# Kernel optimization log

Measured on AMD Instinct MI355X. Metric: run time of the kernel, lower is better.

Reference implementation:

```python
import jax, jax.numpy as jnp
import numpy as np

C, N, B = 16, 65536, 4096  # cases, points per case, batch of case IDs


def _w(key, fan_in, fan_out):
    return jax.random.normal(key, (fan_in, fan_out), dtype=jnp.float32) / np.sqrt(fan_in).astype(np.float32)


def setup_inputs() -> dict:
    key = jax.random.key(0)
    ks = jax.random.split(key, 8)
    pts = jax.random.normal(ks[0], (C, N, 3), dtype=jnp.float32)
    inp = {
        "pts": pts,
        "W1_0": _w(ks[1], 3, 64), "b1_0": jnp.zeros((64,), jnp.float32),
        "W1_1": _w(ks[2], 64, 128), "b1_1": jnp.zeros((128,), jnp.float32),
        "W1_2": _w(ks[3], 128, 512), "b1_2": jnp.zeros((512,), jnp.float32),
        "W2_0": _w(ks[4], 512, 256), "b2_0": jnp.zeros((256,), jnp.float32),
        "W2_1": _w(ks[5], 256, 512), "b2_1": jnp.zeros((512,), jnp.float32),
        "x": jax.random.randint(ks[6], (B,), 0, C, dtype=jnp.int64),
    }
    return inp


def reference(pts, W1_0, b1_0, W1_1, b1_1, W1_2, b1_2, W2_0, b2_0, W2_1, b2_1, x):
    def mlp1(h):  # shared per-point MLP, SiLU after every layer
        h = jax.nn.silu(h @ W1_0 + b1_0)
        h = jax.nn.silu(h @ W1_1 + b1_1)
        h = jax.nn.silu(h @ W1_2 + b1_2)
        return h

    feats = mlp1(pts)                       # [C, N, F1]
    idx = jnp.argmax(feats, axis=1)         # [C, F1] critical-point indices per feature
    # gather critical points (detached in the torch original)
    fixed = jax.lax.stop_gradient(pts[jnp.arange(pts.shape[0])[:, None], idx])  # [C, F1, 3]

    feats2 = mlp1(fixed)                    # [C, F1, F1]
    latent0 = jnp.max(feats2, axis=1)       # [C, F1]

    h = jax.nn.silu(latent0 @ W2_0 + b2_0)  # [C, 256]
    latent = h @ W2_1 + b2_1                # [C, total_modes*ge_features]

    caseID_unit = jax.nn.one_hot(x, latent.shape[0], dtype=latent.dtype)  # [B, C]
    return caseID_unit @ latent             # [B, 512]
```

## Files before the change

### kernel.cpp

```cpp
#include <hip/hip_runtime.h>
#include <math.h>

#define NCASES   16
#define NPTS_BIG 65536
#define F1       512
#define OUT_B    4096

typedef __attribute__((ext_vector_type(8))) short  short8;
typedef __attribute__((ext_vector_type(4))) float  floatx4;

__device__ __forceinline__ float silu_f(float x) {
    return x * __builtin_amdgcn_rcpf(1.0f + __expf(-x));
}

__device__ __forceinline__ unsigned short f2bf(float x) {
    unsigned u = __float_as_uint(x);
    u += 0x7FFFu + ((u >> 16) & 1u);
    return (unsigned short)(u >> 16);
}

__device__ __forceinline__ unsigned enc_f(float x) {
    unsigned u = __float_as_uint(x);
    return (u & 0x80000000u) ? ~u : (u | 0x80000000u);
}
__device__ __forceinline__ float dec_f(unsigned e) {
    unsigned u = (e & 0x80000000u) ? (e ^ 0x80000000u) : ~e;
    return __uint_as_float(u);
}

__global__ void k_init_u64(unsigned long long* a, int n) {
    int i = blockIdx.x * blockDim.x + threadIdx.x;
    if (i < n) a[i] = 0ull;
}

__global__ void k_prep(const float* __restrict__ W11, const float* __restrict__ W12,
                       unsigned short* __restrict__ BbWs, unsigned short* __restrict__ BcWs)
{
    int i = blockIdx.x * 256 + threadIdx.x;
    if (i < 65536) {
        int j = i & 7, l = (i >> 3) & 63, t = i >> 9;
        int KT = t & 3, NT = (t >> 2) & 3, w = t >> 4;
        int k = KT * 32 + (l >> 4) * 8 + j;
        int f = w * 64 + NT * 16 + (l & 15);
        BcWs[i] = f2bf(W12[(size_t)k * 512 + f]);
    }
    if (i < 8192) {
        int j = i & 7, l = (i >> 3) & 63, t = i >> 9;
        int KT = t & 1, w = t >> 1;
        int k = KT * 32 + (l >> 4) * 8 + j;
        int f = w * 16 + (l & 15);
        BbWs[i] = f2bf(W11[(size_t)k * 128 + f]);
    }
}

__global__ __launch_bounds__(512, 2)
void k_mlp1_argmax(const float* __restrict__ pts, int nPts, int chunksPerBlock,
                   const float* __restrict__ W10, const float* __restrict__ b10,
                   const float* __restrict__ b11, const float* __restrict__ b12,
                   const unsigned short* __restrict__ BbWs,
                   const unsigned short* __restrict__ BcWs,
                   unsigned long long* __restrict__ argOut)
{
    const int c   = blockIdx.y;
    const int tid = threadIdx.x;
    const int w   = tid >> 6;
    const int l   = tid & 63;
    const int lm  = l & 15;
    const int q   = l >> 4;

    __shared__ float s_w10[3][64];
    __shared__ float s_b10v[64];
    __shared__ __align__(16) unsigned short s_h0[64][72];
    __shared__ __align__(16) unsigned short s_h1[64][136];

    if (tid < 192) ((float*)s_w10)[tid] = W10[tid];
    if (tid < 64)  s_b10v[tid] = b10[tid];

    short8 Bc[16];
    #pragma unroll
    for (int t = 0; t < 16; ++t)
        Bc[t] = *(const short8*)(BcWs + (size_t)((w * 16 + t) * 64 + l) * 8);
    short8 Bb[2];
    #pragma unroll
    for (int t = 0; t < 2; ++t)
        Bb[t] = *(const short8*)(BbWs + (size_t)((w * 2 + t) * 64 + l) * 8);

    const float bias11 = b11[w * 16 + lm];
    float bias12[4];
    #pragma unroll
    for (int NT = 0; NT < 4; ++NT) bias12[NT] = b12[w * 64 + NT * 16 + lm];

    float    bestv[4];
    unsigned besti[4];
    #pragma unroll
    for (int NT = 0; NT < 4; ++NT) { bestv[NT] = -INFINITY; besti[NT] = 0u; }

    const float* cpts = pts + (size_t)c * nPts * 3;

    for (int ch = 0; ch < chunksPerBlock; ++ch) {
        const int pbase = (blockIdx.x * chunksPerBlock + ch) * 64;
        __syncthreads();

        {
            const int p = tid >> 3, f0 = (tid & 7) * 8;
            const float x = cpts[(size_t)(pbase + p) * 3 + 0];
            const float y = cpts[(size_t)(pbase + p) * 3 + 1];
            const float z = cpts[(size_t)(pbase + p) * 3 + 2];
            short8 hv;
            #pragma unroll
            for (int jj = 0; jj < 8; ++jj) {
                const int f = f0 + jj;
                float v = x * s_w10[0][f] + y * s_w10[1][f] + z * s_w10[2][f] + s_b10v[f];
                hv[jj] = (short)f2bf(silu_f(v));
            }
            *(short8*)&s_h0[p][f0] = hv;
        }
        __syncthreads();

        #pragma unroll
        for (int MT = 0; MT < 4; ++MT) {
            short8 a0 = *(const short8*)&s_h0[MT * 16 + lm][q * 8];
            short8 a1 = *(const short8*)&s_h0[MT * 16 + lm][32 + q * 8];
            floatx4 acc = {0.f, 0.f, 0.f, 0.f};
            acc = __builtin_amdgcn_mfma_f32_16x16x32_bf16(a0, Bb[0], acc, 0, 0, 0);
            acc = __builtin_amdgcn_mfma_f32_16x16x32_bf16(a1, Bb[1], acc, 0, 0, 0);
            #pragma unroll
            for (int r = 0; r < 4; ++r)
                s_h1[MT * 16 + q * 4 + r][w * 16 + lm] = f2bf(silu_f(acc[r] + bias11));
        }
        __syncthreads();

        #pragma unroll
        for (int MT = 0; MT < 4; ++MT) {
            short8 a[4];
            #pragma unroll
            for (int KT = 0; KT < 4; ++KT)
                a[KT] = *(const short8*)&s_h1[MT * 16 + lm][KT * 32 + q * 8];
            #pragma unroll
            for (int NT = 0; NT < 4; ++NT) {
                floatx4 acc = {0.f, 0.f, 0.f, 0.f};
                #pragma unroll
                for (int KT = 0; KT < 4; ++KT)
                    acc = __builtin_amdgcn_mfma_f32_16x16x32_bf16(a[KT], Bc[NT * 4 + KT], acc, 0, 0, 0);
                #pragma unroll
                for (int r = 0; r < 4; ++r) {
                    float v = acc[r];
                    if (v > bestv[NT]) {
                        bestv[NT] = v;
                        besti[NT] = (unsigned)(pbase + MT * 16 + q * 4 + r);
                    }
                }
            }
        }
    }

    #pragma unroll
    for (int NT = 0; NT < 4; ++NT) {
        float v = bestv[NT]; unsigned i = besti[NT];
        #pragma unroll
        for (int m = 16; m <= 32; m <<= 1) {
            float    vo = __shfl_xor(v, m, 64);
            unsigned io = __shfl_xor(i, m, 64);
            if (vo > v || (vo == v && io < i)) { v = vo; i = io; }
        }
        if (q == 0) {
            v += bias12[NT];
            unsigned long long key = ((unsigned long long)enc_f(v) << 32)
                                   | (unsigned long long)(~i);
            atomicMax(&argOut[(size_t)c * 512 + w * 64 + NT * 16 + lm], key);
        }
    }
}

__global__ void k_gather(const float* __restrict__ pts,
                         const unsigned long long* __restrict__ argBuf,
                         float* __restrict__ fixedPts, int nPts)
{
    int id = blockIdx.x * blockDim.x + threadIdx.x;
    if (id >= NCASES * F1) return;
    int c = id >> 9;
    unsigned idx = ~(unsigned)(argBuf[id] & 0xFFFFFFFFull);
    const float* src = pts + ((size_t)c * nPts + idx) * 3;
    float* dst = fixedPts + (size_t)id * 3;
    dst[0] = src[0]; dst[1] = src[1]; dst[2] = src[2];
}

__global__ __launch_bounds__(256)
void k_head(const unsigned long long* __restrict__ argBuf2,
            const float* __restrict__ W20, const float* __restrict__ b20,
            const float* __restrict__ W21, const float* __restrict__ b21,
            float* __restrict__ latent)
{
    const int c = blockIdx.x, tid = threadIdx.x;
    __shared__ float l0[512];
    __shared__ float hh[256];
    l0[tid]       = silu_f(dec_f((unsigned)(argBuf2[(size_t)c * 512 + tid] >> 32)));
    l0[tid + 256] = silu_f(dec_f((unsigned)(argBuf2[(size_t)c * 512 + tid + 256] >> 32)));
    __syncthreads();
    float acc = b20[tid];
    for (int k = 0; k < 512; ++k) acc += l0[k] * W20[(size_t)k * 256 + tid];
    hh[tid] = silu_f(acc);
    __syncthreads();
    #pragma unroll
    for (int r = 0; r < 2; ++r) {
        int f = tid + r * 256;
        float a2 = b21[f];
        for (int k = 0; k < 256; ++k) a2 += hh[k] * W21[(size_t)k * 512 + f];
        latent[(size_t)c * 512 + f] = a2;
    }
}

__global__ void k_scatter(const int* __restrict__ x,
                          const float* __restrict__ latent,
                          float* __restrict__ out)
{
    const int b = blockIdx.x, t = threadIdx.x;
    int cid = x[b];
    const float4* src = (const float4*)(latent + (size_t)cid * 512);
    float4* dst = (float4*)(out + (size_t)b * 512);
    dst[t] = src[t];
}

extern "C" void kernel_launch(void* const* d_in, const int* in_sizes, int n_in,
                              void* d_out, int out_size, void* d_ws, size_t ws_size,
                              hipStream_t stream)
{
    const float* pts = (const float*)d_in[0];
    const float* W10 = (const float*)d_in[1];
    const float* b10 = (const float*)d_in[2];
    const float* W11 = (const float*)d_in[3];
    const float* b11 = (const float*)d_in[4];
    const float* W12 = (const float*)d_in[5];
    const float* b12 = (const float*)d_in[6];
    const float* W20 = (const float*)d_in[7];
    const float* b20 = (const float*)d_in[8];
    const float* W21 = (const float*)d_in[9];
    const float* b21 = (const float*)d_in[10];
    const int*   x   = (const int*)d_in[11];
    float* out = (float*)d_out;

    char* ws = (char*)d_ws;
    unsigned long long* argBuf  = (unsigned long long*)ws;
    unsigned long long* argBuf2 = (unsigned long long*)(ws + 65536);
    float* fixedPts             = (float*)(ws + 131072);
    float* latent               = (float*)(ws + 229376);
    unsigned short* BbWs        = (unsigned short*)(ws + 262144);
    unsigned short* BcWs        = (unsigned short*)(ws + 278528);

    k_init_u64<<<dim3(64), dim3(256), 0, stream>>>(argBuf, NCASES * F1 * 2);

    k_prep<<<dim3(256), dim3(256), 0, stream>>>(W11, W12, BbWs, BcWs);

    k_mlp1_argmax<<<dim3(128, NCASES), dim3(512), 0, stream>>>(
        pts, NPTS_BIG, 8, W10, b10, b11, b12, BbWs, BcWs, argBuf);

    k_gather<<<dim3(32), dim3(256), 0, stream>>>(pts, argBuf, fixedPts, NPTS_BIG);

    k_mlp1_argmax<<<dim3(8, NCASES), dim3(512), 0, stream>>>(
        fixedPts, F1, 1, W10, b10, b11, b12, BbWs, BcWs, argBuf2);

    k_head<<<dim3(NCASES), dim3(256), 0, stream>>>(argBuf2, W20, b20, W21, b21, latent);

    k_scatter<<<dim3(OUT_B), dim3(128), 0, stream>>>(x, latent, out);
}
```

Before: 285.1 us.

## Pack argmax index into mantissa bits, fuse gather and init, use SGPR layer-0 weights

The per-element compare-and-select argmax in the hot loop becomes a plain fmax chain. The low 7 mantissa bits of each accumulator are overwritten with an encoded chunk/row position, and the index is decoded after the loop. The separate gather and init kernels are removed: the second MLP pass reads critical points by index directly, and the argmax buffers are zeroed inside k_prep. Layer-0 weights are held per wave as scalar (uniform) values instead of in LDS, bf16 packing uses a perm instruction, bias11 is preloaded into the MFMA accumulator, and one barrier per chunk is dropped. Truncating 7 mantissa bits slightly coarsens value comparisons, which can change argmax selection between near-tied candidates.

```diff
diff --git a/kernel.cpp b/kernel.cpp
--- a/kernel.cpp
+++ b/kernel.cpp
@@ -13,10 +13,15 @@
     return x * __builtin_amdgcn_rcpf(1.0f + __expf(-x));
 }
 
+__device__ __forceinline__ unsigned f2bf_hi(float x) {
+    unsigned u = __float_as_uint(x);
+    return u + 0x7FFFu + ((u >> 16) & 1u);
+}
 __device__ __forceinline__ unsigned short f2bf(float x) {
-    unsigned u = __float_as_uint(x);
-    u += 0x7FFFu + ((u >> 16) & 1u);
-    return (unsigned short)(u >> 16);
+    return (unsigned short)(f2bf_hi(x) >> 16);
+}
+__device__ __forceinline__ unsigned pk2bf(float lo, float hi) {
+    return __builtin_amdgcn_perm(f2bf_hi(hi), f2bf_hi(lo), 0x07060302u);
 }
 
 __device__ __forceinline__ unsigned enc_f(float x) {
@@ -28,16 +33,17 @@
     return __uint_as_float(u);
 }
 
-__global__ void k_init_u64(unsigned long long* a, int n) {
-    int i = blockIdx.x * blockDim.x + threadIdx.x;
-    if (i < n) a[i] = 0ull;
+__device__ __forceinline__ float sgpr_f(float x) {
+    return __uint_as_float(__builtin_amdgcn_readfirstlane(__float_as_uint(x)));
 }
 
 __global__ void k_prep(const float* __restrict__ W11, const float* __restrict__ W12,
-                       unsigned short* __restrict__ BbWs, unsigned short* __restrict__ BcWs)
+                       unsigned short* __restrict__ BbWs, unsigned short* __restrict__ BcWs,
+                       unsigned long long* __restrict__ argBufs)
 {
     int i = blockIdx.x * 256 + threadIdx.x;
-    if (i < 65536) {
+    if (i < 16384) argBufs[i] = 0ull;
+    {
         int j = i & 7, l = (i >> 3) & 63, t = i >> 9;
         int KT = t & 3, NT = (t >> 2) & 3, w = t >> 4;
         int k = KT * 32 + (l >> 4) * 8 + j;
@@ -55,6 +61,7 @@
 
 __global__ __launch_bounds__(512, 2)
 void k_mlp1_argmax(const float* __restrict__ pts, int nPts, int chunksPerBlock,
+                   const unsigned long long* __restrict__ gatherIdx,
                    const float* __restrict__ W10, const float* __restrict__ b10,
                    const float* __restrict__ b11, const float* __restrict__ b12,
                    const unsigned short* __restrict__ BbWs,
@@ -68,52 +75,64 @@
     const int lm  = l & 15;
     const int q   = l >> 4;
 
-    __shared__ float s_w10[3][64];
-    __shared__ float s_b10v[64];
     __shared__ __align__(16) unsigned short s_h0[64][72];
     __shared__ __align__(16) unsigned short s_h1[64][136];
 
-    if (tid < 192) ((float*)s_w10)[tid] = W10[tid];
-    if (tid < 64)  s_b10v[tid] = b10[tid];
+    const int wf = __builtin_amdgcn_readfirstlane(w);
+
+    float wA0[8], wA1[8], wA2[8], bA[8];
+    #pragma unroll
+    for (int j = 0; j < 8; ++j) {
+        wA0[j] = sgpr_f(W10[  0 + wf * 8 + j]);
+        wA1[j] = sgpr_f(W10[ 64 + wf * 8 + j]);
+        wA2[j] = sgpr_f(W10[128 + wf * 8 + j]);
+        bA[j]  = sgpr_f(b10[       wf * 8 + j]);
+    }
 
     short8 Bc[16];
     #pragma unroll
     for (int t = 0; t < 16; ++t)
-        Bc[t] = *(const short8*)(BcWs + (size_t)((w * 16 + t) * 64 + l) * 8);
+        Bc[t] = *(const short8*)(BcWs + (size_t)((wf * 16 + t) * 64 + l) * 8);
     short8 Bb[2];
     #pragma unroll
     for (int t = 0; t < 2; ++t)
-        Bb[t] = *(const short8*)(BbWs + (size_t)((w * 2 + t) * 64 + l) * 8);
-
-    const float bias11 = b11[w * 16 + lm];
+        Bb[t] = *(const short8*)(BbWs + (size_t)((wf * 2 + t) * 64 + l) * 8);
+
+    const float bias11 = b11[wf * 16 + lm];
     float bias12[4];
     #pragma unroll
-    for (int NT = 0; NT < 4; ++NT) bias12[NT] = b12[w * 64 + NT * 16 + lm];
-
-    float    bestv[4];
-    unsigned besti[4];
-    #pragma unroll
-    for (int NT = 0; NT < 4; ++NT) { bestv[NT] = -INFINITY; besti[NT] = 0u; }
+    for (int NT = 0; NT < 4; ++NT) bias12[NT] = b12[wf * 64 + NT * 16 + lm];
+
+    float bestv[4];
+    #pragma unroll
+    for (int NT = 0; NT < 4; ++NT) bestv[NT] = -INFINITY;
 
     const float* cpts = pts + (size_t)c * nPts * 3;
 
     for (int ch = 0; ch < chunksPerBlock; ++ch) {
         const int pbase = (blockIdx.x * chunksPerBlock + ch) * 64;
-        __syncthreads();
 
         {
-            const int p = tid >> 3, f0 = (tid & 7) * 8;
-            const float x = cpts[(size_t)(pbase + p) * 3 + 0];
-            const float y = cpts[(size_t)(pbase + p) * 3 + 1];
-            const float z = cpts[(size_t)(pbase + p) * 3 + 2];
-            short8 hv;
-            #pragma unroll
-            for (int jj = 0; jj < 8; ++jj) {
-                const int f = f0 + jj;
-                float v = x * s_w10[0][f] + y * s_w10[1][f] + z * s_w10[2][f] + s_b10v[f];
-                hv[jj] = (short)f2bf(silu_f(v));
+            float x, y, z;
+            if (gatherIdx) {
+                unsigned gi = ~(unsigned)(gatherIdx[(size_t)c * 512 + pbase + l] & 0xFFFFFFFFull);
+                const float* sp = cpts + (size_t)gi * 3;
+                x = sp[0]; y = sp[1]; z = sp[2];
+            } else {
+                const float* sp = cpts + (size_t)(pbase + l) * 3;
+                x = sp[0]; y = sp[1]; z = sp[2];
             }
-            *(short8*)&s_h0[p][f0] = hv;
+            float v[8];
+            #pragma unroll
+            for (int j = 0; j < 8; ++j) {
+                float t = fmaf(z, wA2[j], bA[j]);
+                t = fmaf(y, wA1[j], t);
+                t = fmaf(x, wA0[j], t);
+                v[j] = silu_f(t);
+            }
+            uint4 hv = { pk2bf(v[0], v[1]), pk2bf(v[2], v[3]),
+                         pk2bf(v[4], v[5]), pk2bf(v[6], v[7]) };
+            *(uint4*)&s_h0[l][wf * 8] = hv;
         }
         __syncthreads();
 
@@ -121,68 +140,57 @@
         for (int MT = 0; MT < 4; ++MT) {
             short8 a0 = *(const short8*)&s_h0[MT * 16 + lm][q * 8];
             short8 a1 = *(const short8*)&s_h0[MT * 16 + lm][32 + q * 8];
-            floatx4 acc = {0.f, 0.f, 0.f, 0.f};
+            floatx4 acc = {bias11, bias11, bias11, bias11};
             acc = __builtin_amdgcn_mfma_f32_16x16x32_bf16(a0, Bb[0], acc, 0, 0, 0);
             acc = __builtin_amdgcn_mfma_f32_16x16x32_bf16(a1, Bb[1], acc, 0, 0, 0);
             #pragma unroll
             for (int r = 0; r < 4; ++r)
-                s_h1[MT * 16 + q * 4 + r][w * 16 + lm] = f2bf(silu_f(acc[r] + bias11));
+                s_h1[MT * 16 + q * 4 + r][wf * 16 + lm] = f2bf(silu_f(acc[r]));
         }
         __syncthreads();
 
+        const int cb0 = 127 - (ch << 4);
         #pragma unroll
         for (int MT = 0; MT < 4; ++MT) {
             short8 a[4];
             #pragma unroll
             for (int KT = 0; KT < 4; ++KT)
                 a[KT] = *(const short8*)&s_h1[MT * 16 + lm][KT * 32 + q * 8];
+            const int cbM = cb0 - (MT << 2);
             #pragma unroll
             for (int NT = 0; NT < 4; ++NT) {
                 floatx4 acc = {0.f, 0.f, 0.f, 0.f};
                 #pragma unroll
                 for (int KT = 0; KT < 4; ++KT)
                     acc = __builtin_amdgcn_mfma_f32_16x16x32_bf16(a[KT], Bc[NT * 4 + KT], acc, 0, 0, 0);
-                #pragma unroll
-                for (int r = 0; r < 4; ++r) {
-                    float v = acc[r];
-                    if (v > bestv[NT]) {
-                        bestv[NT] = v;
-                        besti[NT] = (unsigned)(pbase + MT * 16 + q * 4 + r);
-                    }
-                }
+                float x0 = __uint_as_float((__float_as_uint(acc[0]) & 0xFFFFFF80u) | (unsigned)(cbM));
+                float x1 = __uint_as_float((__float_as_uint(acc[1]) & 0xFFFFFF80u) | (unsigned)(cbM - 1));
+                float x2 = __uint_as_float((__float_as_uint(acc[2]) & 0xFFFFFF80u) | (unsigned)(cbM - 2));
+                float x3 = __uint_as_float((__float_as_uint(acc[3]) & 0xFFFFFF80u) | (unsigned)(cbM - 3));
+                bestv[NT] = fmaxf(bestv[NT], fmaxf(fmaxf(x0, x1), fmaxf(x2, x3)));
             }
         }
     }
 
     #pragma unroll
     for (int NT = 0; NT < 4; ++NT) {
-        float v = bestv[NT]; unsigned i = besti[NT];
+        unsigned u = __float_as_uint(bestv[NT]);
+        int t = 127 - (int)(u & 127u);
+        unsigned idx = (unsigned)((blockIdx.x * chunksPerBlock + (t >> 4)) * 64
+                                  + ((t >> 2) & 3) * 16 + q * 4 + (t & 3));
+        float v = __uint_as_float(u & 0xFFFFFF80u) + bias12[NT];
         #pragma unroll
         for (int m = 16; m <= 32; m <<= 1) {
             float    vo = __shfl_xor(v, m, 64);
-            unsigned io = __shfl_xor(i, m, 64);
-            if (vo > v || (vo == v && io < i)) { v = vo; i = io; }
+            unsigned io = __shfl_xor(idx, m, 64);
+            if (vo > v || (vo == v && io < idx)) { v = vo; idx = io; }
         }
         if (q == 0) {
-            v += bias12[NT];
             unsigned long long key = ((unsigned long long)enc_f(v) << 32)
-                                   | (unsigned long long)(~i);
-            atomicMax(&argOut[(size_t)c * 512 + w * 64 + NT * 16 + lm], key);
-        }
-    }
-}
-
-__global__ void k_gather(const float* __restrict__ pts,
-                         const unsigned long long* __restrict__ argBuf,
-                         float* __restrict__ fixedPts, int nPts)
-{
-    int id = blockIdx.x * blockDim.x + threadIdx.x;
-    if (id >= NCASES * F1) return;
-    int c = id >> 9;
-    unsigned idx = ~(unsigned)(argBuf[id] & 0xFFFFFFFFull);
-    const float* src = pts + ((size_t)c * nPts + idx) * 3;
-    float* dst = fixedPts + (size_t)id * 3;
-    dst[0] = src[0]; dst[1] = src[1]; dst[2] = src[2];
+                                   | (unsigned long long)(~idx);
+            atomicMax(&argOut[(size_t)c * 512 + wf * 64 + NT * 16 + lm], key);
+        }
+    }
 }
 
 __global__ __launch_bounds__(256)
@@ -242,22 +250,17 @@
     char* ws = (char*)d_ws;
     unsigned long long* argBuf  = (unsigned long long*)ws;
     unsigned long long* argBuf2 = (unsigned long long*)(ws + 65536);
-    float* fixedPts             = (float*)(ws + 131072);
-    float* latent               = (float*)(ws + 229376);
-    unsigned short* BbWs        = (unsigned short*)(ws + 262144);
-    unsigned short* BcWs        = (unsigned short*)(ws + 278528);
-
-    k_init_u64<<<dim3(64), dim3(256), 0, stream>>>(argBuf, NCASES * F1 * 2);
-
-    k_prep<<<dim3(256), dim3(256), 0, stream>>>(W11, W12, BbWs, BcWs);
+    float* latent               = (float*)(ws + 131072);
+    unsigned short* BbWs        = (unsigned short*)(ws + 163840);
+    unsigned short* BcWs        = (unsigned short*)(ws + 180224);
+
+    k_prep<<<dim3(256), dim3(256), 0, stream>>>(W11, W12, BbWs, BcWs, argBuf);
 
     k_mlp1_argmax<<<dim3(128, NCASES), dim3(512), 0, stream>>>(
-        pts, NPTS_BIG, 8, W10, b10, b11, b12, BbWs, BcWs, argBuf);
-
-    k_gather<<<dim3(32), dim3(256), 0, stream>>>(pts, argBuf, fixedPts, NPTS_BIG);
+        pts, NPTS_BIG, 8, nullptr, W10, b10, b11, b12, BbWs, BcWs, argBuf);
 
     k_mlp1_argmax<<<dim3(8, NCASES), dim3(512), 0, stream>>>(
-        fixedPts, F1, 1, W10, b10, b11, b12, BbWs, BcWs, argBuf2);
+        pts, NPTS_BIG, 1, argBuf, W10, b10, b11, b12, BbWs, BcWs, argBuf2);
 
     k_head<<<dim3(NCASES), dim3(256), 0, stream>>>(argBuf2, W20, b20, W21, b21, latent);
 
```

Result: slower. 314.3 us (+10.2%).
